# Kernel tuning notes

Measured on AMD Instinct MI355X. Metric: run time of the kernel, lower is better.

The kernel has to match this reference:

```python
import jax, jax.numpy as jnp
import numpy as np

B, C, H, W = 4, 256, 64, 64
N = H * W


def setup_inputs() -> dict:
    key = jax.random.key(0)
    k1, k2, k3, k4, k5 = jax.random.split(key, 5)
    energy = jax.random.normal(k1, (B, N, N), dtype=jnp.float32)
    x = jax.random.normal(k2, (B, C, H, W), dtype=jnp.float32)
    # 1x1 conv params (kernel is [C_out, C_in] after squeezing the 1x1 spatial dims)
    fan = 1.0 / np.sqrt(C)
    value_w = jax.random.uniform(k3, (C, C), dtype=jnp.float32, minval=-fan, maxval=fan)
    value_b = jax.random.uniform(k4, (C,), dtype=jnp.float32, minval=-fan, maxval=fan)
    # nn.Parameter(torch.zeros(1)) -> use small random scalar so output is non-trivial
    gamma = jax.random.normal(k5, (1,), dtype=jnp.float32) * 0.1
    return {"energy": energy, "x": x, "value_w": value_w, "value_b": value_b, "gamma": gamma}


def reference(energy, x, value_w, value_b, gamma):
    # softmax over last dim of the [B, N, N] score matrix (dropout in eval mode = identity)
    attention = jax.nn.softmax(energy, axis=-1)  # [B, N, N]
    # 1x1 conv: per-pixel channel mixing
    value = jnp.einsum('bchw,oc->bohw', x, value_w) + value_b[None, :, None, None]
    value = value.reshape(x.shape[0], -1, N)  # [B, C, N]
    # out[b,c,m] = sum_n value[b,c,n] * attention[b,m,n]  (bmm with attention^T)
    out = jnp.einsum('bcn,bmn->bcm', value, attention)
    out = out.reshape(x.shape)  # [B, C, H, W]
    return gamma[0] * out + 2.0 * x
```

## Files before the change

### kernel.cpp

```cpp
#include <hip/hip_runtime.h>

#define Nn 4096
#define Cc 256
#define NN2 ((size_t)Nn * Nn)

typedef __attribute__((ext_vector_type(8))) short bf16x8;
typedef __attribute__((ext_vector_type(4))) short bf16x4;
typedef __attribute__((ext_vector_type(4))) float f32x4;

#define LDSBAR() do { \
    asm volatile("s_waitcnt lgkmcnt(0)" ::: "memory"); \
    __builtin_amdgcn_s_barrier(); \
} while (0)

__device__ __forceinline__ unsigned short f2bf(float f) {
    union { float f; unsigned u; } v; v.f = f;
    unsigned r = v.u + 0x7FFF + ((v.u >> 16) & 1);
    return (unsigned short)(r >> 16);
}

__device__ __forceinline__ bf16x8 pack2(const float4& a, const float4& b) {
    bf16x8 o;
    o[0] = (short)f2bf(a.x); o[1] = (short)f2bf(a.y);
    o[2] = (short)f2bf(a.z); o[3] = (short)f2bf(a.w);
    o[4] = (short)f2bf(b.x); o[5] = (short)f2bf(b.y);
    o[6] = (short)f2bf(b.z); o[7] = (short)f2bf(b.w);
    return o;
}

__device__ __forceinline__ void expstore4(const float4& a,
                                          unsigned short* dst, float& sacc) {
    const float s0 = __expf(a.x), s1 = __expf(a.y), s2 = __expf(a.z), s3 = __expf(a.w);
    sacc += (s0 + s1) + (s2 + s3);
    bf16x4 o;
    o[0] = (short)f2bf(s0); o[1] = (short)f2bf(s1);
    o[2] = (short)f2bf(s2); o[3] = (short)f2bf(s3);
    *(bf16x4*)dst = o;
}

__global__ __launch_bounds__(256) void value_gemm(
    const float* __restrict__ X, const float* __restrict__ W,
    const float* __restrict__ bias, unsigned short* __restrict__ Vout)
{
    __shared__ float Xs[256][33];

    const int t = threadIdx.x;
    const int b  = blockIdx.x >> 7;
    const int n0 = (blockIdx.x & 127) << 5;
    const int wave = t >> 6, lane = t & 63;
    const int lrow = lane & 15, lq = lane >> 4;

    const float* Xb = X + (size_t)b * Cc * Nn + n0;

    {
        const int r0 = t >> 3, c4 = (t & 7) << 2;
        #pragma unroll
        for (int i = 0; i < 8; ++i) {
            const int r = r0 + i * 32;
            const float4 v = *(const float4*)(Xb + (size_t)r * Nn + c4);
            Xs[r][c4 + 0] = v.x; Xs[r][c4 + 1] = v.y;
            Xs[r][c4 + 2] = v.z; Xs[r][c4 + 3] = v.w;
        }
    }
    __syncthreads();

    f32x4 acc[4][2] = {};

    #pragma unroll 2
    for (int k0 = 0; k0 < Cc; k0 += 32) {
        bf16x8 af[4];
        #pragma unroll
        for (int ci = 0; ci < 4; ++ci) {
            const float* wp = W + (size_t)(wave * 64 + ci * 16 + lrow) * Cc + k0 + lq * 8;
            af[ci] = pack2(*(const float4*)wp, *(const float4*)(wp + 4));
        }
        bf16x8 bp[2];
        #pragma unroll
        for (int mi = 0; mi < 2; ++mi) {
            const int n = mi * 16 + lrow;
            bf16x8 o;
            #pragma unroll
            for (int j = 0; j < 8; ++j) o[j] = (short)f2bf(Xs[k0 + lq * 8 + j][n]);
            bp[mi] = o;
        }
        #pragma unroll
        for (int ci = 0; ci < 4; ++ci)
            #pragma unroll
            for (int mi = 0; mi < 2; ++mi)
                acc[ci][mi] = __builtin_amdgcn_mfma_f32_16x16x32_bf16(
                    af[ci], bp[mi], acc[ci][mi], 0, 0, 0);
    }

    #pragma unroll
    for (int ci = 0; ci < 4; ++ci) {
        #pragma unroll
        for (int rr = 0; rr < 4; ++rr) {
            const int o = wave * 64 + ci * 16 + lq * 4 + rr;
            const float bo = bias[o];
            #pragma unroll
            for (int mi = 0; mi < 2; ++mi) {
                const int n = n0 + mi * 16 + lrow;
                Vout[((size_t)(b * Cc + o)) * Nn + n] = f2bf(acc[ci][mi][rr] + bo);
            }
        }
    }
}

__global__ __launch_bounds__(512, 4) void attn_gemm(
    const unsigned short* __restrict__ V, const float* __restrict__ E,
    const float* __restrict__ X, const float* __restrict__ gamma,
    float* __restrict__ Out)
{
    __shared__ unsigned short Bexp[2][32 * 64];
    __shared__ float sum_lds[32];

    const int t = threadIdx.x;
    const int wave = t >> 6, lane = t & 63;
    const int lrow = lane & 15, lq = lane >> 4;
    const int l7 = lrow & 7;
    const int blk = blockIdx.x;
    const int b  = (blk & 7) >> 1;
    const int m0 = (((blk >> 3) << 1) | (blk & 1)) << 5;

    const int erow = t >> 4, eg = t & 15;
    const float* ep = E + (size_t)b * NN2 + (size_t)(m0 + erow) * Nn + eg * 4;
    const int ss = erow * 64 + (((eg >> 1) ^ (erow & 7)) << 3) + ((eg & 1) << 2);
    unsigned short* const bst0 = &Bexp[0][ss];
    unsigned short* const bst1 = &Bexp[1][ss];

    const unsigned short* vbase = V + (size_t)(b * Cc + wave * 32) * Nn;
    int voff[2];
    voff[0] = lrow * Nn + lq * 8;
    voff[1] = (16 + lrow) * Nn + lq * 8;

    f32x4 acc[2][2] = {};
    float sacc = 0.f;

    float4 eE0, eE1;
    bf16x8 vA[4], vB[4];

    eE0 = *(const float4*)(ep);
    eE1 = *(const float4*)(ep + 64);
    #pragma unroll
    for (int kk = 0; kk < 2; ++kk)
        #pragma unroll
        for (int ci = 0; ci < 2; ++ci)
            vA[kk * 2 + ci] = *(const bf16x8*)(vbase + voff[ci] + kk * 32);
    expstore4(eE0, bst0, sacc);
    eE0 = *(const float4*)(ep + 128);
    LDSBAR();

    for (int k = 0; k < 64; k += 2) {
        {
            bf16x8 bfr[2][2];
            #pragma unroll
            for (int kk = 0; kk < 2; ++kk)
                #pragma unroll
                for (int mi = 0; mi < 2; ++mi) {
                    const int rm = mi * 16 + lrow;
                    bfr[kk][mi] = *(const bf16x8*)&Bexp[0][rm * 64 + (((kk * 4 + lq) ^ l7) << 3)];
                }
            const int kv = (k + 1) << 6;
            #pragma unroll
            for (int kk = 0; kk < 2; ++kk)
                #pragma unroll
                for (int ci = 0; ci < 2; ++ci)
                    vB[kk * 2 + ci] = *(const bf16x8*)(vbase + voff[ci] + kv + kk * 32);
            expstore4(eE1, bst1, sacc);
            eE1 = *(const float4*)(ep + (((k + 3) & 63) << 6));
            __builtin_amdgcn_s_setprio(1);
            #pragma unroll
            for (int ci = 0; ci < 2; ++ci)
                #pragma unroll
                for (int mi = 0; mi < 2; ++mi)
                    #pragma unroll
                    for (int kk = 0; kk < 2; ++kk)
                        acc[ci][mi] = __builtin_amdgcn_mfma_f32_16x16x32_bf16(
                            vA[kk * 2 + ci], bfr[kk][mi], acc[ci][mi], 0, 0, 0);
            __builtin_amdgcn_s_setprio(0);
            LDSBAR();
        }
        {
            bf16x8 bfr[2][2];
            #pragma unroll
            for (int kk = 0; kk < 2; ++kk)
                #pragma unroll
                for (int mi = 0; mi < 2; ++mi) {
                    const int rm = mi * 16 + lrow;
                    bfr[kk][mi] = *(const bf16x8*)&Bexp[1][rm * 64 + (((kk * 4 + lq) ^ l7) << 3)];
                }
            const int kv = ((k + 2) & 63) << 6;
            #pragma unroll
            for (int kk = 0; kk < 2; ++kk)
                #pragma unroll
                for (int ci = 0; ci < 2; ++ci)
                    vA[kk * 2 + ci] = *(const bf16x8*)(vbase + voff[ci] + kv + kk * 32);
            if (k != 62) {
                expstore4(eE0, bst0, sacc);
                eE0 = *(const float4*)(ep + (((k + 4) & 63) << 6));
            }
            __builtin_amdgcn_s_setprio(1);
            #pragma unroll
            for (int ci = 0; ci < 2; ++ci)
                #pragma unroll
                for (int mi = 0; mi < 2; ++mi)
                    #pragma unroll
                    for (int kk = 0; kk < 2; ++kk)
                        acc[ci][mi] = __builtin_amdgcn_mfma_f32_16x16x32_bf16(
                            vB[kk * 2 + ci], bfr[kk][mi], acc[ci][mi], 0, 0, 0);
            __builtin_amdgcn_s_setprio(0);
            LDSBAR();
        }
    }

    {
        float s = sacc;
        s += __shfl_xor(s, 1);
        s += __shfl_xor(s, 2);
        s += __shfl_xor(s, 4);
        s += __shfl_xor(s, 8);
        if (eg == 0) sum_lds[erow] = s;
    }
    __syncthreads();

    const float g = gamma[0];
    #pragma unroll
    for (int mi = 0; mi < 2; ++mi) {
        const int mloc = mi * 16 + lrow;
        const float scale = g / sum_lds[mloc];
        const int m = m0 + mloc;
        #pragma unroll
        for (int ci = 0; ci < 2; ++ci) {
            #pragma unroll
            for (int rr = 0; rr < 4; ++rr) {
                const int c = wave * 32 + ci * 16 + lq * 4 + rr;
                const size_t off = ((size_t)(b * Cc + c)) * Nn + m;
                Out[off] = scale * acc[ci][mi][rr] + 2.0f * X[off];
            }
        }
    }
}

extern "C" void kernel_launch(void* const* d_in, const int* in_sizes, int n_in,
                              void* d_out, int out_size, void* d_ws, size_t ws_size,
                              hipStream_t stream) {
    const float* energy  = (const float*)d_in[0];
    const float* x       = (const float*)d_in[1];
    const float* value_w = (const float*)d_in[2];
    const float* value_b = (const float*)d_in[3];
    const float* gamma   = (const float*)d_in[4];
    float* out = (float*)d_out;
    unsigned short* Vws = (unsigned short*)d_ws;

    value_gemm<<<512, 256, 0, stream>>>(x, value_w, value_b, Vws);
    attn_gemm<<<512, 512, 0, stream>>>(Vws, energy, x, gamma, out);
}
```

Before: 455.3 us.

## Stream energy tiles into LDS via global_load_lds with a 4-stage ring

Replaces the register-staged float4 loads of the energy matrix with direct global-to-LDS DMA (global_load_lds) into a four-slot raw fp32 ring, prefetching three k-steps ahead. Each step then reads its slot from LDS, exponentiates and packs to bf16, while vmcnt waits are tuned per stage. The intent is deeper prefetch of the dominant energy stream with fewer VGPRs and less issue overhead. In exchange it adds 32KB of LDS per block, which may cut occupancy below the 4-block launch bound, plus an extra LDS round trip.

```diff
diff --git a/kernel.cpp b/kernel.cpp
--- a/kernel.cpp
+++ b/kernel.cpp
@@ -8,10 +8,9 @@
 typedef __attribute__((ext_vector_type(4))) short bf16x4;
 typedef __attribute__((ext_vector_type(4))) float f32x4;
 
-#define LDSBAR() do { \
-    asm volatile("s_waitcnt lgkmcnt(0)" ::: "memory"); \
-    __builtin_amdgcn_s_barrier(); \
-} while (0)
+#define GLOAD(src, dst) __builtin_amdgcn_global_load_lds( \
+    (const __attribute__((address_space(1))) void*)(src), \
+    (__attribute__((address_space(3))) void*)(dst), 16, 0, 0)
 
 __device__ __forceinline__ unsigned short f2bf(float f) {
     union { float f; unsigned u; } v; v.f = f;
@@ -111,6 +110,7 @@
     const float* __restrict__ X, const float* __restrict__ gamma,
     float* __restrict__ Out)
 {
+    __shared__ float Eraw[4][32 * 64];
     __shared__ unsigned short Bexp[2][32 * 64];
     __shared__ float sum_lds[32];
 
@@ -123,95 +123,85 @@
     const int m0 = (((blk >> 3) << 1) | (blk & 1)) << 5;
 
     const int erow = t >> 4, eg = t & 15;
-    const float* ep = E + (size_t)b * NN2 + (size_t)(m0 + erow) * Nn + eg * 4;
+    const int eslot = erow * 64 + eg * 4;
     const int ss = erow * 64 + (((eg >> 1) ^ (erow & 7)) << 3) + ((eg & 1) << 2);
-    unsigned short* const bst0 = &Bexp[0][ss];
-    unsigned short* const bst1 = &Bexp[1][ss];
+
+    const int drow = wave * 4 + (lane >> 4);
+    const float* egbase = E + (size_t)b * NN2 + (size_t)(m0 + drow) * Nn + ((lane & 15) << 2);
 
     const unsigned short* vbase = V + (size_t)(b * Cc + wave * 32) * Nn;
-    int voff[2];
-    voff[0] = lrow * Nn + lq * 8;
-    voff[1] = (16 + lrow) * Nn + lq * 8;
+    const int voff0 = lrow * Nn + lq * 8;
+    const int voff1 = (16 + lrow) * Nn + lq * 8;
 
     f32x4 acc[2][2] = {};
     float sacc = 0.f;
-
-    float4 eE0, eE1;
     bf16x8 vA[4], vB[4];
 
-    eE0 = *(const float4*)(ep);
-    eE1 = *(const float4*)(ep + 64);
-    #pragma unroll
-    for (int kk = 0; kk < 2; ++kk)
-        #pragma unroll
-        for (int ci = 0; ci < 2; ++ci)
-            vA[kk * 2 + ci] = *(const bf16x8*)(vbase + voff[ci] + kk * 32);
-    expstore4(eE0, bst0, sacc);
-    eE0 = *(const float4*)(ep + 128);
-    LDSBAR();
-
-    for (int k = 0; k < 64; k += 2) {
-        {
-            bf16x8 bfr[2][2];
-            #pragma unroll
-            for (int kk = 0; kk < 2; ++kk)
-                #pragma unroll
-                for (int mi = 0; mi < 2; ++mi) {
-                    const int rm = mi * 16 + lrow;
-                    bfr[kk][mi] = *(const bf16x8*)&Bexp[0][rm * 64 + (((kk * 4 + lq) ^ l7) << 3)];
-                }
-            const int kv = (k + 1) << 6;
-            #pragma unroll
-            for (int kk = 0; kk < 2; ++kk)
-                #pragma unroll
-                for (int ci = 0; ci < 2; ++ci)
-                    vB[kk * 2 + ci] = *(const bf16x8*)(vbase + voff[ci] + kv + kk * 32);
-            expstore4(eE1, bst1, sacc);
-            eE1 = *(const float4*)(ep + (((k + 3) & 63) << 6));
-            __builtin_amdgcn_s_setprio(1);
-            #pragma unroll
-            for (int ci = 0; ci < 2; ++ci)
-                #pragma unroll
-                for (int mi = 0; mi < 2; ++mi)
-                    #pragma unroll
-                    for (int kk = 0; kk < 2; ++kk)
-                        acc[ci][mi] = __builtin_amdgcn_mfma_f32_16x16x32_bf16(
-                            vA[kk * 2 + ci], bfr[kk][mi], acc[ci][mi], 0, 0, 0);
-            __builtin_amdgcn_s_setprio(0);
-            LDSBAR();
-        }
-        {
-            bf16x8 bfr[2][2];
-            #pragma unroll
-            for (int kk = 0; kk < 2; ++kk)
-                #pragma unroll
-                for (int mi = 0; mi < 2; ++mi) {
-                    const int rm = mi * 16 + lrow;
-                    bfr[kk][mi] = *(const bf16x8*)&Bexp[1][rm * 64 + (((kk * 4 + lq) ^ l7) << 3)];
-                }
-            const int kv = ((k + 2) & 63) << 6;
-            #pragma unroll
-            for (int kk = 0; kk < 2; ++kk)
-                #pragma unroll
-                for (int ci = 0; ci < 2; ++ci)
-                    vA[kk * 2 + ci] = *(const bf16x8*)(vbase + voff[ci] + kv + kk * 32);
-            if (k != 62) {
-                expstore4(eE0, bst0, sacc);
-                eE0 = *(const float4*)(ep + (((k + 4) & 63) << 6));
-            }
-            __builtin_amdgcn_s_setprio(1);
-            #pragma unroll
-            for (int ci = 0; ci < 2; ++ci)
-                #pragma unroll
-                for (int mi = 0; mi < 2; ++mi)
-                    #pragma unroll
-                    for (int kk = 0; kk < 2; ++kk)
-                        acc[ci][mi] = __builtin_amdgcn_mfma_f32_16x16x32_bf16(
-                            vB[kk * 2 + ci], bfr[kk][mi], acc[ci][mi], 0, 0, 0);
-            __builtin_amdgcn_s_setprio(0);
-            LDSBAR();
-        }
-    }
+    GLOAD(egbase,            &Eraw[0][wave * 256]);
+    GLOAD(egbase + (1 << 6), &Eraw[1][wave * 256]);
+    GLOAD(egbase + (2 << 6), &Eraw[2][wave * 256]);
+    vA[0] = *(const bf16x8*)(vbase + voff0);
+    vA[1] = *(const bf16x8*)(vbase + voff1);
+    vA[2] = *(const bf16x8*)(vbase + voff0 + 32);
+    vA[3] = *(const bf16x8*)(vbase + voff1 + 32);
+    asm volatile("s_waitcnt vmcnt(6)" ::: "memory");
+    __builtin_amdgcn_s_barrier();
+    {
+        const float4 ev = *(const float4*)&Eraw[0][eslot];
+        expstore4(ev, &Bexp[0][ss], sacc);
+    }
+
+#define STEP(T, Vc, Vn, DO_DMA, DO_EXP, DO_VL, VMC)                            \
+    {                                                                          \
+        asm volatile("s_waitcnt lgkmcnt(0)" ::: "memory");                     \
+        __builtin_amdgcn_s_barrier();                                          \
+        if (DO_VL) {                                                           \
+            const int kv = ((T) + 1) << 6;                                     \
+            Vn[0] = *(const bf16x8*)(vbase + voff0 + kv);                      \
+            Vn[1] = *(const bf16x8*)(vbase + voff1 + kv);                      \
+            Vn[2] = *(const bf16x8*)(vbase + voff0 + kv + 32);                 \
+            Vn[3] = *(const bf16x8*)(vbase + voff1 + kv + 32);                 \
+        }                                                                      \
+        if (DO_DMA) {                                                          \
+            GLOAD(egbase + (((T) + 3) << 6), &Eraw[((T) + 3) & 3][wave * 256]);\
+        }                                                                      \
+        bf16x8 bfr[2][2];                                                      \
+        _Pragma("unroll")                                                      \
+        for (int kk = 0; kk < 2; ++kk)                                         \
+            _Pragma("unroll")                                                  \
+            for (int mi = 0; mi < 2; ++mi) {                                   \
+                const int rm = mi * 16 + lrow;                                 \
+                bfr[kk][mi] = *(const bf16x8*)                                 \
+                    &Bexp[(T) & 1][rm * 64 + (((kk * 4 + lq) ^ l7) << 3)];     \
+            }                                                                  \
+        asm volatile("s_waitcnt vmcnt(" #VMC ")" ::: "memory");                \
+        if (DO_EXP) {                                                          \
+            const float4 ev = *(const float4*)&Eraw[((T) + 1) & 3][eslot];     \
+            expstore4(ev, &Bexp[((T) + 1) & 1][ss], sacc);                     \
+        }                                                                      \
+        __builtin_amdgcn_s_setprio(1);                                         \
+        _Pragma("unroll")                                                      \
+        for (int ci = 0; ci < 2; ++ci)                                         \
+            _Pragma("unroll")                                                  \
+            for (int mi = 0; mi < 2; ++mi) {                                   \
+                acc[ci][mi] = __builtin_amdgcn_mfma_f32_16x16x32_bf16(         \
+                    Vc[0 * 2 + ci], bfr[0][mi], acc[ci][mi], 0, 0, 0);         \
+                acc[ci][mi] = __builtin_amdgcn_mfma_f32_16x16x32_bf16(         \
+                    Vc[1 * 2 + ci], bfr[1][mi], acc[ci][mi], 0, 0, 0);         \
+            }                                                                  \
+        __builtin_amdgcn_s_setprio(0);                                         \
+    }
+
+    #pragma unroll 1
+    for (int k = 0; k < 60; k += 2) {
+        STEP(k,     vA, vB, 1, 1, 1, 6);
+        STEP(k + 1, vB, vA, 1, 1, 1, 6);
+    }
+    STEP(60, vA, vB, 1, 1, 1, 6);
+    STEP(61, vB, vA, 0, 1, 1, 0);
+    STEP(62, vA, vB, 0, 1, 1, 0);
+    STEP(63, vB, vA, 0, 0, 0, 0);
+#undef STEP
 
     {
         float s = sacc;
```

After: 455.5 us. No clear change (+0.0%).
